# Performance work log

Measured on AMD Instinct MI355X. Metric: run time of the kernel, lower is better.

The kernel has to match this reference:

```python
import math
import jax, jax.numpy as jnp
import numpy as np

B, L, ENC_IN, TFEAT = 32, 1024, 21, 4
DM, EXP = 256, 2
DI = DM * EXP            # 512 d_inner
DST = 64                 # d_state (= configs.d_ff in this repo)
HD = 64                  # headdim
NH = DI // HD            # 8 heads
DC = 4                   # d_conv
NL = 4                   # n_layers
PRED = 192
CO = 21
Q = 64                   # SSD chunk length
DIP = 2 * DI + 2 * DST + NH    # in_proj out dim (z, xBC, dt)
CONVD = DI + 2 * DST           # depthwise-conv channels


def silu(x):
    return x * jax.nn.sigmoid(x)


def positional_embedding(l, d):
    pe = np.zeros((l, d), np.float32)
    pos = np.arange(l, dtype=np.float32)[:, None]
    div = np.exp(np.arange(0, d, 2, dtype=np.float32) * (-math.log(10000.0) / d))
    pe[:, 0::2] = np.sin(pos * div)
    pe[:, 1::2] = np.cos(pos * div)
    return jnp.asarray(pe)


def layernorm(x, g, b):
    m = jnp.mean(x, -1, keepdims=True)
    v = jnp.mean((x - m) ** 2, -1, keepdims=True)
    return (x - m) * jax.lax.rsqrt(v + 1e-5) * g + b


def segsum(x):
    # x: (..., T) -> (..., T, T); out[i,j] = sum_{j<k<=i} x[k], -inf above diagonal
    T = x.shape[-1]
    xx = jnp.broadcast_to(x[..., :, None], (*x.shape, T))
    m1 = jnp.tril(jnp.ones((T, T), bool), -1)
    xs = jnp.cumsum(jnp.where(m1, xx, 0.0), axis=-2)
    m2 = jnp.tril(jnp.ones((T, T), bool), 0)
    return jnp.where(m2, xs, -jnp.inf)


def ssd(X, A, Bm, Cm):
    # chunked SSD (Mamba2). X: (b,l,h,p) = x*dt; A: (b,l,h) = dt*(-exp(A_log)); B,C: (b,l,n)
    b, l, h, p = X.shape
    c = l // Q
    Xc = X.reshape(b, c, Q, h, p)
    Ac = A.reshape(b, c, Q, h).transpose(0, 3, 1, 2)      # (b,h,c,q)
    Bc = Bm.reshape(b, c, Q, -1)
    Cc = Cm.reshape(b, c, Q, -1)
    Acum = jnp.cumsum(Ac, -1)                              # (b,h,c,q)
    Lmat = jnp.exp(segsum(Ac))                             # (b,h,c,q,q)
    Y_diag = jnp.einsum('bcqn,bcsn,bhcqs,bcshp->bcqhp', Cc, Bc, Lmat, Xc)
    decay_states = jnp.exp(Acum[..., -1:] - Acum)          # (b,h,c,q)
    states = jnp.einsum('bcqn,bhcq,bcqhp->bchpn', Bc, decay_states, Xc)
    states = jnp.concatenate([jnp.zeros_like(states[:, :1]), states], axis=1)  # (b,c+1,h,p,n)
    decay_chunk = jnp.exp(segsum(jnp.pad(Acum[..., -1], ((0, 0), (0, 0), (1, 0)))))  # (b,h,c+1,c+1)
    new_states = jnp.einsum('bhzc,bchpn->bzhpn', decay_chunk, states)
    states = new_states[:, :-1]                            # (b,c,h,p,n) entering each chunk
    sdo = jnp.exp(Acum)                                    # (b,h,c,q)
    Y_off = jnp.einsum('bcqn,bchpn,bhcq->bcqhp', Cc, states, sdo)
    return (Y_diag + Y_off).reshape(b, l, h, p)


def mamba2(x, Wi, cw, cb, dtb, Alog, Dp, gw, Wo):
    b, l, _ = x.shape
    zxbcdt = x @ Wi.T                                      # (b,l,DIP)
    z = zxbcdt[..., :DI]
    xBC = zxbcdt[..., DI:DI + CONVD]
    dt = zxbcdt[..., DI + CONVD:]
    # causal depthwise conv (kernel DC) + SiLU
    xp = jnp.pad(xBC, ((0, 0), (DC - 1, 0), (0, 0)))
    xBC = silu(sum(xp[:, k:k + l, :] * cw[:, k] for k in range(DC)) + cb)
    xs = xBC[..., :DI].reshape(b, l, NH, HD)
    Bm = xBC[..., DI:DI + DST]
    Cm = xBC[..., DI + DST:]
    dt = jax.nn.softplus(dt + dtb)                         # (b,l,NH)
    A = -jnp.exp(Alog)                                     # (NH,)
    y = ssd(xs * dt[..., None], dt * A, Bm, Cm) + xs * Dp[:, None]
    y = y.reshape(b, l, DI)
    y = y * silu(z)                                        # gated RMSNorm
    y = y * jax.lax.rsqrt(jnp.mean(y * y, -1, keepdims=True) + 1e-5) * gw
    return y @ Wo.T


def setup_inputs():
    key = jax.random.key(0)
    ks = jax.random.split(key, 16)
    x_enc = jax.random.normal(ks[0], (B, L, ENC_IN), jnp.float32)
    x_mark_enc = jax.random.normal(ks[1], (B, L, TFEAT), jnp.float32)
    x_dec = jax.random.normal(ks[2], (B, 240, ENC_IN), jnp.float32)
    x_mark_dec = jax.random.normal(ks[3], (B, 240, TFEAT), jnp.float32)
    token_w = jax.random.normal(ks[4], (DM, ENC_IN, 3), jnp.float32) * 0.1
    temb_w = jax.random.normal(ks[5], (DM, TFEAT), jnp.float32) * 0.1
    ln_g = jnp.ones((NL, DM), jnp.float32)
    ln_b = jnp.zeros((NL, DM), jnp.float32)
    in_proj_w = jax.random.normal(ks[6], (NL, DIP, DM), jnp.float32) * (DM ** -0.5)
    conv_w = jax.random.normal(ks[7], (NL, CONVD, DC), jnp.float32) * 0.2
    conv_b = jnp.zeros((NL, CONVD), jnp.float32)
    dt_bias = jax.random.normal(ks[8], (NL, NH), jnp.float32) * 0.5
    A_log = jnp.log(jax.random.uniform(ks[9], (NL, NH), jnp.float32, 1.0, 16.0))
    Dskip = jnp.ones((NL, NH), jnp.float32)
    gnorm_w = jnp.ones((NL, DI), jnp.float32)
    out_proj_w = jax.random.normal(ks[10], (NL, DM, DI), jnp.float32) * (DI ** -0.5)
    head_w = jax.random.normal(ks[11], (CO, DM), jnp.float32) * (DM ** -0.5)
    return dict(x_enc=x_enc, x_mark_enc=x_mark_enc, x_dec=x_dec, x_mark_dec=x_mark_dec,
                token_w=token_w, temb_w=temb_w, ln_g=ln_g, ln_b=ln_b,
                in_proj_w=in_proj_w, conv_w=conv_w, conv_b=conv_b, dt_bias=dt_bias,
                A_log=A_log, Dskip=Dskip, gnorm_w=gnorm_w, out_proj_w=out_proj_w,
                head_w=head_w)


def reference(x_enc, x_mark_enc, x_dec, x_mark_dec, token_w, temb_w, ln_g, ln_b,
              in_proj_w, conv_w, conv_b, dt_bias, A_log, Dskip, gnorm_w, out_proj_w, head_w):
    # instance normalization (detached stats)
    mean = jax.lax.stop_gradient(jnp.mean(x_enc, 1, keepdims=True))
    xz = x_enc - mean
    std = jax.lax.stop_gradient(jnp.sqrt(jnp.var(xz, axis=1, keepdims=True) + 1e-5))
    xz = xz / std
    l = xz.shape[1]
    # token embedding: circular-pad Conv1d(enc_in->d_model, k=3)
    xpad = jnp.pad(xz, ((0, 0), (1, 1), (0, 0)), mode='wrap')
    tok = sum(jnp.einsum('blc,dc->bld', xpad[:, k:k + l], token_w[:, :, k]) for k in range(3))
    h = tok + positional_embedding(l, DM)[None] + x_mark_enc @ temb_w.T
    for i in range(NL):
        y = mamba2(h, in_proj_w[i], conv_w[i], conv_b[i], dt_bias[i], A_log[i],
                   Dskip[i], gnorm_w[i], out_proj_w[i])
        h = layernorm(h + y, ln_g[i], ln_b[i])
    out = h @ head_w.T
    out = out * std + mean
    return out[:, -PRED:, :]
```

## Files before the change

### kernel.cpp

```cpp
#include <hip/hip_runtime.h>
#include <hip/hip_bf16.h>


typedef unsigned short ushort_t;
typedef unsigned int uint_t;
typedef __attribute__((ext_vector_type(8))) short short8;
typedef __attribute__((ext_vector_type(4))) float f32x4;
typedef __attribute__((ext_vector_type(4))) ushort_t ushort4_t;

__device__ __forceinline__ float b2f(ushort_t u) {
    uint_t v = ((uint_t)u) << 16;
    return __builtin_bit_cast(float, v);
}
__device__ __forceinline__ ushort_t f2b(float f) {
    uint_t u = __builtin_bit_cast(uint_t, f);
    uint_t r = (u + 0x7FFFu + ((u >> 16) & 1u)) >> 16;
    return (ushort_t)r;
}
__device__ __forceinline__ uint_t cvt_pk2(float a, float b) {
    uint_t r;
    asm("v_cvt_pk_bf16_f32 %0, %1, %2" : "=v"(r) : "v"(a), "v"(b));
    return r;
}
__device__ __forceinline__ float silu_f(float x) {
    return x / (1.f + __expf(-x));
}
__device__ __forceinline__ void gl_lds16(const ushort_t* g, ushort_t* l) {
    __builtin_amdgcn_global_load_lds(
        (const __attribute__((address_space(1))) unsigned int*)g,
        (__attribute__((address_space(3))) unsigned int*)l, 16, 0, 0);
}

__global__ __launch_bounds__(256) void cvt_pad_ip(const float* __restrict__ in,
        ushort_t* __restrict__ out) {
    int i = blockIdx.x * 256 + threadIdx.x;
    if (i >= 4 * 1280 * 256) return;
    int layer = i / (1280 * 256);
    int rem = i - layer * 1280 * 256;
    int n = rem >> 8, k = rem & 255;
    out[i] = (n < 1160) ? f2b(in[(size_t)layer * 1160 * 256 + n * 256 + k]) : (ushort_t)0;
}
__global__ __launch_bounds__(256) void cvt_wop(const float* __restrict__ in,
        const float* __restrict__ gw, ushort_t* __restrict__ out) {
    int i = blockIdx.x * 256 + threadIdx.x;
    int layer = i >> 17;
    int c = i & 511;
    out[i] = f2b(in[i] * gw[layer * 512 + c]);
}
__global__ __launch_bounds__(256) void cvt_convw(const float* __restrict__ in,
        float* __restrict__ out) {
    int i = blockIdx.x * 256 + threadIdx.x;
    if (i >= 10240) return;
    int layer = i / 2560;
    int rem = i - layer * 2560;
    int k = rem / 640, ch = rem - k * 640;
    out[i] = in[layer * 2560 + ch * 4 + k];
}

__global__ __launch_bounds__(256) void pe_kernel(float* __restrict__ pe) {
    int l = blockIdx.x, d = threadIdx.x;
    float div = __expf((float)(d & ~1) * (-9.210340371976184f / 256.0f));
    float arg = (float)l * div;
    pe[l * 256 + d] = (d & 1) ? cosf(arg) : sinf(arg);
}

__global__ __launch_bounds__(256) void stats_kernel(const float* __restrict__ xe,
        float* __restrict__ meanb, float* __restrict__ stdb, float* __restrict__ rstdb) {
    int bi = blockIdx.x;
    int b = bi / 21, c = bi - b * 21;
    int tid = threadIdx.x;
    float s = 0.f, s2 = 0.f;
    for (int l = tid; l < 1024; l += 256) {
        float v = xe[(b * 1024 + l) * 21 + c];
        s += v; s2 += v * v;
    }
    __shared__ float r1[4], r2[4];
    for (int o = 32; o > 0; o >>= 1) { s += __shfl_down(s, o, 64); s2 += __shfl_down(s2, o, 64); }
    if ((tid & 63) == 0) { r1[tid >> 6] = s; r2[tid >> 6] = s2; }
    __syncthreads();
    if (tid == 0) {
        float S = r1[0] + r1[1] + r1[2] + r1[3];
        float S2 = r2[0] + r2[1] + r2[2] + r2[3];
        float m = S * (1.f / 1024.f);
        float var = S2 * (1.f / 1024.f) - m * m;
        float sd = sqrtf(var + 1e-5f);
        meanb[bi] = m; stdb[bi] = sd; rstdb[bi] = 1.f / sd;
    }
}

__global__ __launch_bounds__(256) void embed3_kernel(const float* __restrict__ xe,
        const float* __restrict__ xm, const float* __restrict__ tokw,
        const float* __restrict__ tembw, const float* __restrict__ pe,
        const float* __restrict__ meanb, const float* __restrict__ rstdb,
        float* __restrict__ h, ushort_t* __restrict__ hbf) {
    int blk = blockIdx.x;
    int b = blk >> 4, t = blk & 15;
    int l0 = t * 64;
    int tid = threadIdx.x;
    __shared__ float xw[66][22];
    __shared__ float xmw[64][4];
    __shared__ float mn[21], rs[21];
    if (tid < 21) { mn[tid] = meanb[b * 21 + tid]; rs[tid] = rstdb[b * 21 + tid]; }
    float twr[63];
    {
        const float* tp = tokw + tid * 63;
        #pragma unroll
        for (int i = 0; i < 63; i++) twr[i] = tp[i];
    }
    float tbr[4];
    #pragma unroll
    for (int k = 0; k < 4; k++) tbr[k] = tembw[tid * 4 + k];
    __syncthreads();
    for (int i = tid; i < 1386; i += 256) {
        int row = i / 21, c = i - row * 21;
        int gl = (l0 - 1 + row + 1024) & 1023;
        xw[row][c] = (xe[(size_t)(b * 1024 + gl) * 21 + c] - mn[c]) * rs[c];
    }
    {
        int row = tid >> 2, c = tid & 3;
        xmw[row][c] = xm[(size_t)(b * 1024 + l0 + row) * 4 + c];
    }
    __syncthreads();
    int d = tid;
    float acc2 = 0.f, acc1 = 0.f;
    for (int r = 0; r < 66; r++) {
        float s0 = 0.f, s1 = 0.f, s2 = 0.f;
        #pragma unroll
        for (int c = 0; c < 21; c++) {
            float xv = xw[r][c];
            s0 += xv * twr[c * 3 + 0];
            s1 += xv * twr[c * 3 + 1];
            s2 += xv * twr[c * 3 + 2];
        }
        if (r >= 2) {
            int li = r - 2;
            float acc = acc2 + s2 + pe[(size_t)(l0 + li) * 256 + d];
            #pragma unroll
            for (int k = 0; k < 4; k++) acc += xmw[li][k] * tbr[k];
            size_t o = (size_t)(b * 1024 + l0 + li) * 256 + d;
            h[o] = acc;
            hbf[o] = f2b(acc);
        }
        acc2 = acc1 + s1;
        acc1 = s0;
    }
}

template<int KDIM>
__device__ __forceinline__ void gemm128_main(const ushort_t* __restrict__ Ab,
        const ushort_t* __restrict__ Wb, ushort_t* sA, ushort_t* sW,
        f32x4 (&acc)[16], int m0, int n0) {
    int tid = threadIdx.x;
    int w = tid >> 6, lane = tid & 63;
    int wm = w >> 1, wn = w & 1;
    int rr = lane & 15, quad = lane >> 4;
    int srow0 = w * 32 + (lane >> 2);
    int skk = (lane & 3) * 8;
    int sl0 = w * 1024 + lane * 8;
    for (int k0 = 0; k0 < KDIM; k0 += 64) {
        __syncthreads();
        #pragma unroll
        for (int p = 0; p < 2; p++) {
            #pragma unroll
            for (int j = 0; j < 2; j++) {
                int row = srow0 + j * 16;
                int koff = k0 + p * 32 + skk;
                gl_lds16(Ab + (size_t)(m0 + row) * KDIM + koff, &sA[p * 4096 + sl0 + j * 512]);
                gl_lds16(Wb + (size_t)(n0 + row) * KDIM + koff, &sW[p * 4096 + sl0 + j * 512]);
            }
        }
        __syncthreads();
        #pragma unroll
        for (int p = 0; p < 2; p++) {
            short8 a[4], b[4];
            #pragma unroll
            for (int i = 0; i < 4; i++)
                a[i] = *(const short8*)&sA[p * 4096 + (wm * 64 + i * 16 + rr) * 32 + quad * 8];
            #pragma unroll
            for (int j = 0; j < 4; j++)
                b[j] = *(const short8*)&sW[p * 4096 + (wn * 64 + j * 16 + rr) * 32 + quad * 8];
            #pragma unroll
            for (int i = 0; i < 4; i++)
                #pragma unroll
                for (int j = 0; j < 4; j++)
                    acc[i * 4 + j] = __builtin_amdgcn_mfma_f32_16x16x32_bf16(a[i], b[j], acc[i * 4 + j], 0, 0, 0);
        }
    }
}

__global__ __launch_bounds__(256) void gemm_ip(const ushort_t* __restrict__ A,
        const ushort_t* __restrict__ W, ushort_t* __restrict__ zbuf,
        ushort_t* __restrict__ xbuf) {
    int g = blockIdx.x;
    int xcd = g & 7, s = g >> 3;
    int sq = s / 10;
    int tn = s - sq * 10;
    int tm = (sq << 3) | xcd;
    int m0 = tm * 128, n0 = tn * 128;
    __shared__ ushort_t sA[8192], sW[8192];
    f32x4 acc[16];
    #pragma unroll
    for (int i = 0; i < 16; i++) acc[i] = (f32x4){0.f, 0.f, 0.f, 0.f};
    gemm128_main<256>(A, W, sA, sW, acc, m0, n0);
    int lane = threadIdx.x & 63, w = threadIdx.x >> 6;
    int wm = w >> 1, wn = w & 1;
    int rr = lane & 15, quad = lane >> 4;
    #pragma unroll
    for (int i = 0; i < 4; i++) {
        int mrow = m0 + wm * 64 + i * 16 + quad * 4;
        #pragma unroll
        for (int j = 0; j < 4; j++) {
            int n = n0 + wn * 64 + j * 16 + rr;
            uint_t u01 = cvt_pk2(acc[i * 4 + j][0], acc[i * 4 + j][1]);
            uint_t u23 = cvt_pk2(acc[i * 4 + j][2], acc[i * 4 + j][3]);
            ushort_t vs[4] = {(ushort_t)u01, (ushort_t)(u01 >> 16),
                              (ushort_t)u23, (ushort_t)(u23 >> 16)};
            #pragma unroll
            for (int r2 = 0; r2 < 4; r2++) {
                if (n < 512) zbuf[(size_t)(mrow + r2) * 512 + n] = vs[r2];
                else if (n < 1160) xbuf[(size_t)(mrow + r2) * 704 + (n - 512)] = vs[r2];
            }
        }
    }
}

__global__ __launch_bounds__(256) void gemm_og(const ushort_t* __restrict__ Yb,
        const ushort_t* __restrict__ Zb, const ushort_t* __restrict__ Wb,
        float* __restrict__ h, ushort_t* __restrict__ hbf,
        const float* __restrict__ lng, const float* __restrict__ lnb) {
    int m0 = blockIdx.x * 32;
    int tid = threadIdx.x;
    int w = tid >> 6, lane = tid & 63;
    int wm = w >> 1, wn = w & 1;
    int rr = lane & 15, quad = lane >> 4;
    __shared__ ushort_t sA[2048];
    __shared__ ushort_t sW[16384];
    __shared__ float gssq[32];
    __shared__ float rsum[32][2], rssq[32][2];

    int arow = tid >> 3;
    int akk = (tid & 7) * 8;
    const ushort_t* yrow = Yb + (size_t)(m0 + arow) * 512 + akk;
    const ushort_t* zrow = Zb + (size_t)(m0 + arow) * 512 + akk;
    ushort_t* adst = &sA[((tid & 7) >> 2) * 1024 + arow * 32 + (tid & 3) * 8];

    f32x4 acc[8];
    #pragma unroll
    for (int j = 0; j < 8; j++) acc[j] = (f32x4){0.f, 0.f, 0.f, 0.f};
    float ssqr = 0.f;

    short8 y0 = *(const short8*)(yrow);
    short8 z0 = *(const short8*)(zrow);

    for (int k0 = 0; k0 < 512; k0 += 64) {
        __syncthreads();
        short8 ga;
        {
            uint_t* gau = (uint_t*)&ga;
            #pragma unroll
            for (int jj = 0; jj < 8; jj += 2) {
                float g0 = b2f(((ushort_t*)&y0)[jj]) * silu_f(b2f(((ushort_t*)&z0)[jj]));
                float g1 = b2f(((ushort_t*)&y0)[jj + 1]) * silu_f(b2f(((ushort_t*)&z0)[jj + 1]));
                ssqr += g0 * g0 + g1 * g1;
                gau[jj >> 1] = cvt_pk2(g0, g1);
            }
        }
        *(short8*)adst = ga;
        if (k0 + 64 < 512) {
            y0 = *(const short8*)(yrow + k0 + 64);
            z0 = *(const short8*)(zrow + k0 + 64);
        }
        #pragma unroll
        for (int p = 0; p < 2; p++) {
            #pragma unroll
            for (int j = 0; j < 4; j++)
                gl_lds16(Wb + (size_t)(w * 64 + j * 16 + (lane >> 2)) * 512
                             + k0 + p * 32 + (lane & 3) * 8,
                         &sW[p * 8192 + w * 2048 + j * 512 + lane * 8]);
        }
        __syncthreads();
        #pragma unroll
        for (int p = 0; p < 2; p++) {
            short8 a = *(const short8*)&sA[p * 1024 + (wm * 16 + rr) * 32 + quad * 8];
            #pragma unroll
            for (int j = 0; j < 8; j++) {
                short8 bv = *(const short8*)&sW[p * 8192 + (wn * 128 + j * 16 + rr) * 32 + quad * 8];
                acc[j] = __builtin_amdgcn_mfma_f32_16x16x32_bf16(a, bv, acc[j], 0, 0, 0);
            }
        }
    }

    ssqr += __shfl_xor(ssqr, 1, 64);
    ssqr += __shfl_xor(ssqr, 2, 64);
    ssqr += __shfl_xor(ssqr, 4, 64);
    if ((tid & 7) == 0) gssq[arow] = ssqr;
    __syncthreads();

    float gl[8], bl[8];
    #pragma unroll
    for (int j = 0; j < 8; j++) {
        int col = wn * 128 + j * 16 + rr;
        gl[j] = lng[col]; bl[j] = lnb[col];
    }
    #pragma unroll
    for (int r2 = 0; r2 < 4; r2++) {
        int rowl = wm * 16 + quad * 4 + r2;
        float rmsv = rsqrtf(gssq[rowl] * (1.f / 512.f) + 1e-5f);
        size_t gbase = (size_t)(m0 + rowl) * 256;
        float s = 0.f, s2 = 0.f;
        #pragma unroll
        for (int j = 0; j < 8; j++) {
            int col = wn * 128 + j * 16 + rr;
            float xv = h[gbase + col] + acc[j][r2] * rmsv;
            acc[j][r2] = xv;
            s += xv; s2 += xv * xv;
        }
        #pragma unroll
        for (int o = 1; o < 16; o <<= 1) {
            s += __shfl_xor(s, o, 64);
            s2 += __shfl_xor(s2, o, 64);
        }
        if (rr == 0) { rsum[rowl][wn] = s; rssq[rowl][wn] = s2; }
    }
    __syncthreads();
    #pragma unroll
    for (int r2 = 0; r2 < 4; r2++) {
        int rowl = wm * 16 + quad * 4 + r2;
        float S = rsum[rowl][0] + rsum[rowl][1];
        float S2 = rssq[rowl][0] + rssq[rowl][1];
        float mu = S * (1.f / 256.f);
        float var = S2 * (1.f / 256.f) - mu * mu;
        float rstd = rsqrtf(var + 1e-5f);
        size_t gbase = (size_t)(m0 + rowl) * 256;
        #pragma unroll
        for (int j = 0; j < 8; j++) {
            int col = wn * 128 + j * 16 + rr;
            float o = (acc[j][r2] - mu) * rstd * gl[j] + bl[j];
            h[gbase + col] = o;
            hbf[gbase + col] = f2b(o);
        }
    }
}

__global__ __launch_bounds__(256) void conv_kernel(const ushort_t* __restrict__ xbuf,
        const float* __restrict__ cwt, const float* __restrict__ cb,
        const float* __restrict__ dtb, ushort_t* __restrict__ xc,
        float* __restrict__ dts) {
    if (blockIdx.x >= 2560) {
        int r = (blockIdx.x - 2560) * 256 + threadIdx.x;
        short8 dv = *(const short8*)(xbuf + (size_t)r * 704 + 640);
        #pragma unroll
        for (int j = 0; j < 8; j++) {
            float x = b2f(((ushort_t*)&dv)[j]) + dtb[j];
            dts[(size_t)r * 8 + j] = (x > 20.f) ? x : log1pf(__expf(x));
        }
        return;
    }
    int idx = blockIdx.x * 256 + threadIdx.x;
    int g = idx % 80;
    int rt = idx / 80;
    int ch0 = g * 8;
    int b = rt >> 8;
    int l0 = (rt & 255) << 2;
    float wgt[4][8];
    #pragma unroll
    for (int k = 0; k < 4; k++) {
        float4 w0 = *(const float4*)(cwt + k * 640 + ch0);
        float4 w1 = *(const float4*)(cwt + k * 640 + ch0 + 4);
        wgt[k][0] = w0.x; wgt[k][1] = w0.y; wgt[k][2] = w0.z; wgt[k][3] = w0.w;
        wgt[k][4] = w1.x; wgt[k][5] = w1.y; wgt[k][6] = w1.z; wgt[k][7] = w1.w;
    }
    float bias[8];
    {
        float4 b0 = *(const float4*)(cb + ch0);
        float4 b1 = *(const float4*)(cb + ch0 + 4);
        bias[0] = b0.x; bias[1] = b0.y; bias[2] = b0.z; bias[3] = b0.w;
        bias[4] = b1.x; bias[5] = b1.y; bias[6] = b1.z; bias[7] = b1.w;
    }
    short8 xr[7];
    const ushort_t* base = xbuf + (size_t)(b * 1024 + l0) * 704 + ch0;
    #pragma unroll
    for (int i = 0; i < 7; i++) {
        int ll = l0 - 3 + i;
        if (ll >= 0) xr[i] = *(const short8*)(base + (ptrdiff_t)(i - 3) * 704);
        else         xr[i] = (short8){0, 0, 0, 0, 0, 0, 0, 0};
    }
    #pragma unroll
    for (int lo = 0; lo < 4; lo++) {
        float acc[8];
        #pragma unroll
        for (int j = 0; j < 8; j++) acc[j] = bias[j];
        #pragma unroll
        for (int k = 0; k < 4; k++) {
            #pragma unroll
            for (int j = 0; j < 8; j++)
                acc[j] += b2f(((ushort_t*)&xr[lo + k])[j]) * wgt[k][j];
        }
        short8 o;
        #pragma unroll
        for (int j = 0; j < 8; j++) ((ushort_t*)&o)[j] = f2b(silu_f(acc[j]));
        *(short8*)(xc + (size_t)(b * 1024 + l0 + lo) * 640 + ch0) = o;
    }
}

__global__ __launch_bounds__(256) void ssd_stateA4(const ushort_t* __restrict__ xc,
        const float* __restrict__ dts, const float* __restrict__ alog,
        float* __restrict__ stbuf, float* __restrict__ acbuf) {
    int idx = blockIdx.x;
    int bh = idx >> 2, grp = idx & 3;
    int b = bh >> 3, h = bh & 7;
    float Ah = -__expf(alog[h]);
    int tid = threadIdx.x;
    int q = tid >> 2, pb = (tid & 3) * 16;
    int w = tid >> 6, lane = tid & 63;
    int rr = lane & 15, quad = lane >> 4, qb = w * 16;

    __shared__ ushort_t Bt[64][68], Xt[64][68];
    __shared__ float dec_s[64];
    __shared__ float ad_sh;

    float T[4][4];
    #pragma unroll
    for (int t = 0; t < 4; t++)
        #pragma unroll
        for (int r2 = 0; r2 < 4; r2++) T[t][r2] = 0.f;

    ushort_t bv[16], xv[16];
    float d_pf = 0.f;
    {
        int chunk = grp * 4;
        int l0 = chunk * 64;
        const ushort_t* xrow = xc + (size_t)(b * 1024 + l0 + q) * 640;
        *(short8*)&bv[0] = *(const short8*)(xrow + 512 + pb);
        *(short8*)&bv[8] = *(const short8*)(xrow + 512 + pb + 8);
        *(short8*)&xv[0] = *(const short8*)(xrow + h * 64 + pb);
        *(short8*)&xv[8] = *(const short8*)(xrow + h * 64 + pb + 8);
        if (tid < 64)
            d_pf = dts[(size_t)(b * 1024 + l0 + tid) * 8 + h];
    }

    for (int c4 = 0; c4 < 4; c4++) {
        int chunk = grp * 4 + c4;
        size_t cidx = (size_t)bh * 16 + chunk;
        #pragma unroll
        for (int j = 0; j < 16; j++) Xt[pb + j][q] = xv[j];
        if (tid < 64) {
            float d = d_pf;
            float a = d * Ah;
            #pragma unroll
            for (int off = 1; off < 64; off <<= 1) {
                float t = __shfl_up(a, off, 64);
                if (tid >= off) a += t;
            }
            acbuf[cidx * 64 + tid] = a;
            float tot = __shfl(a, 63, 64);
            dec_s[tid] = __expf(tot - a) * d;
            if (tid == 0) ad_sh = __expf(tot);
        }
        __syncthreads();
        {
            float dq = dec_s[q];
            #pragma unroll
            for (int j = 0; j < 16; j += 2) {
                uint_t u = cvt_pk2(b2f(bv[j]) * dq, b2f(bv[j + 1]) * dq);
                Bt[pb + j][q] = (ushort_t)u;
                Bt[pb + j + 1][q] = (ushort_t)(u >> 16);
            }
        }
        if (c4 < 3) {
            int l0n = (chunk + 1) * 64;
            const ushort_t* xrow = xc + (size_t)(b * 1024 + l0n + q) * 640;
            *(short8*)&bv[0] = *(const short8*)(xrow + 512 + pb);
            *(short8*)&bv[8] = *(const short8*)(xrow + 512 + pb + 8);
            *(short8*)&xv[0] = *(const short8*)(xrow + h * 64 + pb);
            *(short8*)&xv[8] = *(const short8*)(xrow + h * 64 + pb + 8);
            if (tid < 64)
                d_pf = dts[(size_t)(b * 1024 + l0n + tid) * 8 + h];
        }
        __syncthreads();
        f32x4 acc[4];
        #pragma unroll
        for (int t = 0; t < 4; t++) acc[t] = (f32x4){0.f, 0.f, 0.f, 0.f};
        #pragma unroll
        for (int ks = 0; ks < 2; ks++) {
            short8 a = *(const short8*)(&Bt[qb + rr][ks * 32 + quad * 8]);
            #pragma unroll
            for (int t = 0; t < 4; t++) {
                short8 bb = *(const short8*)(&Xt[t * 16 + rr][ks * 32 + quad * 8]);
                acc[t] = __builtin_amdgcn_mfma_f32_16x16x32_bf16(a, bb, acc[t], 0, 0, 0);
            }
        }
        {
            float ad = ad_sh;
            #pragma unroll
            for (int t = 0; t < 4; t++)
                #pragma unroll
                for (int r2 = 0; r2 < 4; r2++)
                    T[t][r2] = ad * T[t][r2] + acc[t][r2];
        }
        __syncthreads();
    }
    float* sb = stbuf + (size_t)idx * 4096;
    #pragma unroll
    for (int t = 0; t < 4; t++) {
        int p = t * 16 + rr;
        #pragma unroll
        for (int r2 = 0; r2 < 4; r2++)
            sb[(qb + quad * 4 + r2) * 64 + p] = T[t][r2];
    }
}

__global__ __launch_bounds__(256) void ssd_outBC4(const ushort_t* __restrict__ xc,
        const float* __restrict__ dts, const float* __restrict__ acbuf,
        const float* __restrict__ dsk, const float* __restrict__ stbuf,
        ushort_t* __restrict__ ybuf) {
    int idx = blockIdx.x;
    int bh = idx >> 2, grp = idx & 3;
    int b = bh >> 3, h = bh & 7;
    float Dh = dsk[h];
    int tid = threadIdx.x;
    int q = tid >> 2, pb = (tid & 3) * 16;
    int w = tid >> 6, lane = tid & 63;
    int rr = lane & 15, quad = lane >> 4, qb = w * 16;

    __shared__ ushort_t Cs[64][68], Bs[64][68], Xt[64][68],
                        Bt[64][68], Shi[64][68], Slo[64][68];
    ushort_t (&Gs)[64][68] = Bs;
    __shared__ float acum_s[64], dtq_s[64], ea_s[64], dec_s[64];
    __shared__ float ad_sh;

    float S[4][4];
    #pragma unroll
    for (int t = 0; t < 4; t++)
        #pragma unroll
        for (int r2 = 0; r2 < 4; r2++) S[t][r2] = 0.f;
    for (int g = 0; g < grp; g++) {
        float Ag = 1.f;
        #pragma unroll
        for (int c = 0; c < 4; c++)
            Ag *= __expf(acbuf[((size_t)bh * 16 + g * 4 + c) * 64 + 63]);
        const float* s0 = stbuf + (size_t)(bh * 4 + g) * 4096;
        #pragma unroll
        for (int t = 0; t < 4; t++) {
            int p = t * 16 + rr;
            #pragma unroll
            for (int r2 = 0; r2 < 4; r2++)
                S[t][r2] = Ag * S[t][r2] + s0[(qb + quad * 4 + r2) * 64 + p];
        }
    }

    ushort_t bv[16], cv[16], xv[16];
    float a_pf = 0.f, d_pf = 0.f;
    {
        int chunk = grp * 4;
        int l0 = chunk * 64;
        const ushort_t* xrow = xc + (size_t)(b * 1024 + l0 + q) * 640;
        *(short8*)&bv[0] = *(const short8*)(xrow + 512 + pb);
        *(short8*)&bv[8] = *(const short8*)(xrow + 512 + pb + 8);
        *(short8*)&cv[0] = *(const short8*)(xrow + 576 + pb);
        *(short8*)&cv[8] = *(const short8*)(xrow + 576 + pb + 8);
        *(short8*)&xv[0] = *(const short8*)(xrow + h * 64 + pb);
        *(short8*)&xv[8] = *(const short8*)(xrow + h * 64 + pb + 8);
        if (tid < 64) {
            size_t cidx = (size_t)bh * 16 + chunk;
            a_pf = acbuf[cidx * 64 + tid];
            d_pf = dts[(size_t)(b * 1024 + l0 + tid) * 8 + h];
        }
    }

    int qq0 = qb + quad * 4;
    for (int c4 = 0; c4 < 4; c4++) {
        int chunk = grp * 4 + c4;
        int l0 = chunk * 64;
        *(short8*)&Bs[q][pb]     = *(const short8*)&bv[0];
        *(short8*)&Bs[q][pb + 8] = *(const short8*)&bv[8];
        *(short8*)&Cs[q][pb]     = *(const short8*)&cv[0];
        *(short8*)&Cs[q][pb + 8] = *(const short8*)&cv[8];
        #pragma unroll
        for (int j = 0; j < 16; j++) Xt[pb + j][q] = xv[j];
        if (tid < 64) {
            float a = a_pf;
            acum_s[tid] = a;
            ea_s[tid] = __expf(a);
            float d = d_pf;
            dtq_s[tid] = d;
            float tot = __shfl(a, 63, 64);
            dec_s[tid] = __expf(tot - a) * d;
            if (tid == 0) ad_sh = __expf(tot);
        }
        #pragma unroll
        for (int t = 0; t < 4; t++) {
            int p = t * 16 + rr;
            uint_t h01 = cvt_pk2(S[t][0], S[t][1]);
            uint_t h23 = cvt_pk2(S[t][2], S[t][3]);
            float l0r = S[t][0] - b2f((ushort_t)h01);
            float l1r = S[t][1] - b2f((ushort_t)(h01 >> 16));
            float l2r = S[t][2] - b2f((ushort_t)h23);
            float l3r = S[t][3] - b2f((ushort_t)(h23 >> 16));
            uint_t lo01 = cvt_pk2(l0r, l1r);
            uint_t lo23 = cvt_pk2(l2r, l3r);
            *(uint2*)&Shi[p][qq0] = make_uint2(h01, h23);
            *(uint2*)&Slo[p][qq0] = make_uint2(lo01, lo23);
        }
        __syncthreads();

        {
            float dq = dec_s[q];
            #pragma unroll
            for (int j = 0; j < 16; j += 2) {
                uint_t u = cvt_pk2(b2f(bv[j]) * dq, b2f(bv[j + 1]) * dq);
                Bt[pb + j][q] = (ushort_t)u;
                Bt[pb + j + 1][q] = (ushort_t)(u >> 16);
            }
        }
        if (c4 < 3) {
            int l0n = (chunk + 1) * 64;
            const ushort_t* xrow = xc + (size_t)(b * 1024 + l0n + q) * 640;
            *(short8*)&bv[0] = *(const short8*)(xrow + 512 + pb);
            *(short8*)&bv[8] = *(const short8*)(xrow + 512 + pb + 8);
            *(short8*)&cv[0] = *(const short8*)(xrow + 576 + pb);
            *(short8*)&cv[8] = *(const short8*)(xrow + 576 + pb + 8);
            *(short8*)&xv[0] = *(const short8*)(xrow + h * 64 + pb);
            *(short8*)&xv[8] = *(const short8*)(xrow + h * 64 + pb + 8);
            if (tid < 64) {
                size_t cidxn = (size_t)bh * 16 + chunk + 1;
                a_pf = acbuf[cidxn * 64 + tid];
                d_pf = dts[(size_t)(b * 1024 + l0n + tid) * 8 + h];
            }
        }
        uint_t gp01[4], gp23[4];
        {
            f32x4 g[4];
            #pragma unroll
            for (int t = 0; t < 4; t++) g[t] = (f32x4){0.f, 0.f, 0.f, 0.f};
            #pragma unroll
            for (int ks = 0; ks < 2; ks++) {
                short8 a = *(const short8*)(&Cs[qb + rr][ks * 32 + quad * 8]);
                #pragma unroll
                for (int t = 0; t < 4; t++) {
                    short8 bb = *(const short8*)(&Bs[t * 16 + rr][ks * 32 + quad * 8]);
                    g[t] = __builtin_amdgcn_mfma_f32_16x16x32_bf16(a, bb, g[t], 0, 0, 0);
                }
            }
            #pragma unroll
            for (int t = 0; t < 4; t++) {
                int s = t * 16 + rr;
                float as = acum_s[s], dss = dtq_s[s];
                float vv[4];
                #pragma unroll
                for (int r2 = 0; r2 < 4; r2++) {
                    int qq = qq0 + r2;
                    vv[r2] = (s <= qq) ? g[t][r2] * __expf(acum_s[qq] - as) * dss : 0.f;
                }
                gp01[t] = cvt_pk2(vv[0], vv[1]);
                gp23[t] = cvt_pk2(vv[2], vv[3]);
            }
        }
        __syncthreads();
        #pragma unroll
        for (int t = 0; t < 4; t++) {
            int s = t * 16 + rr;
            Gs[qq0][s]     = (ushort_t)gp01[t];
            Gs[qq0 + 1][s] = (ushort_t)(gp01[t] >> 16);
            Gs[qq0 + 2][s] = (ushort_t)gp23[t];
            Gs[qq0 + 3][s] = (ushort_t)(gp23[t] >> 16);
        }
        __syncthreads();

        f32x4 aD[4], aO[4];
        #pragma unroll
        for (int t = 0; t < 4; t++) { aD[t] = (f32x4){0.f,0.f,0.f,0.f}; aO[t] = (f32x4){0.f,0.f,0.f,0.f}; }
        #pragma unroll
        for (int ks = 0; ks < 2; ks++) {
            short8 ga = *(const short8*)(&Gs[qb + rr][ks * 32 + quad * 8]);
            short8 ca = *(const short8*)(&Cs[qb + rr][ks * 32 + quad * 8]);
            #pragma unroll
            for (int t = 0; t < 4; t++) {
                short8 xb = *(const short8*)(&Xt[t * 16 + rr][ks * 32 + quad * 8]);
                short8 sh = *(const short8*)(&Shi[t * 16 + rr][ks * 32 + quad * 8]);
                short8 sl = *(const short8*)(&Slo[t * 16 + rr][ks * 32 + quad * 8]);
                aD[t] = __builtin_amdgcn_mfma_f32_16x16x32_bf16(ga, xb, aD[t], 0, 0, 0);
                aO[t] = __builtin_amdgcn_mfma_f32_16x16x32_bf16(ca, sh, aO[t], 0, 0, 0);
                aO[t] = __builtin_amdgcn_mfma_f32_16x16x32_bf16(ca, sl, aO[t], 0, 0, 0);
            }
        }
        {
            f32x4 acc[4];
            #pragma unroll
            for (int t = 0; t < 4; t++) acc[t] = (f32x4){0.f, 0.f, 0.f, 0.f};
            #pragma unroll
            for (int ks = 0; ks < 2; ks++) {
                short8 a = *(const short8*)(&Bt[qb + rr][ks * 32 + quad * 8]);
                #pragma unroll
                for (int t = 0; t < 4; t++) {
                    short8 bb = *(const short8*)(&Xt[t * 16 + rr][ks * 32 + quad * 8]);
                    acc[t] = __builtin_amdgcn_mfma_f32_16x16x32_bf16(a, bb, acc[t], 0, 0, 0);
                }
            }
            #pragma unroll
            for (int t = 0; t < 4; t++) {
                int p = t * 16 + rr;
                float yv[4];
                #pragma unroll
                for (int r2 = 0; r2 < 4; r2++) {
                    int qq = qq0 + r2;
                    yv[r2] = aD[t][r2] + ea_s[qq] * aO[t][r2] + Dh * b2f(Xt[p][qq]);
                }
                uint_t u01 = cvt_pk2(yv[0], yv[1]);
                uint_t u23 = cvt_pk2(yv[2], yv[3]);
                size_t base = (size_t)(b * 1024 + l0 + qq0) * 512 + h * 64 + p;
                ybuf[base]        = (ushort_t)u01;
                ybuf[base + 512]  = (ushort_t)(u01 >> 16);
                ybuf[base + 1024] = (ushort_t)u23;
                ybuf[base + 1536] = (ushort_t)(u23 >> 16);
            }
            float ad = ad_sh;
            #pragma unroll
            for (int t = 0; t < 4; t++)
                #pragma unroll
                for (int r2 = 0; r2 < 4; r2++)
                    S[t][r2] = ad * S[t][r2] + acc[t][r2];
        }
        __syncthreads();
    }
}

__global__ __launch_bounds__(256) void head_kernel(const float* __restrict__ h,
        const float* __restrict__ hw, const float* __restrict__ stdb,
        const float* __restrict__ meanb, float* __restrict__ out) {
    int blk = blockIdx.x;
    int b = blk / 192, t = blk - b * 192;
    int l = 832 + t;
    int tid = threadIdx.x;
    __shared__ float hr[256];
    hr[tid] = h[(size_t)(b * 1024 + l) * 256 + tid];
    __syncthreads();
    if (tid < 21) {
        float acc = 0.f;
        for (int k = 0; k < 256; k++) acc += hr[k] * hw[tid * 256 + k];
        out[(size_t)blk * 21 + tid] = acc * stdb[b * 21 + tid] + meanb[b * 21 + tid];
    }
}

extern "C" void kernel_launch(void* const* d_in, const int* in_sizes, int n_in,
                              void* d_out, int out_size, void* d_ws, size_t ws_size,
                              hipStream_t stream) {
    const float* x_enc  = (const float*)d_in[0];
    const float* x_mark = (const float*)d_in[1];
    const float* tokw   = (const float*)d_in[4];
    const float* tembw  = (const float*)d_in[5];
    const float* ln_g   = (const float*)d_in[6];
    const float* ln_b   = (const float*)d_in[7];
    const float* ipw    = (const float*)d_in[8];
    const float* cw     = (const float*)d_in[9];
    const float* cb     = (const float*)d_in[10];
    const float* dtb    = (const float*)d_in[11];
    const float* alog   = (const float*)d_in[12];
    const float* dsk    = (const float*)d_in[13];
    const float* gw     = (const float*)d_in[14];
    const float* opw    = (const float*)d_in[15];
    const float* hw     = (const float*)d_in[16];
    float* out = (float*)d_out;

    char* w = (char*)d_ws;
    size_t off = 0;
    auto alloc = [&](size_t bytes) -> void* {
        void* p = w + off;
        off += (bytes + 255) & ~(size_t)255;
        return p;
    };
    float* meanb  = (float*)alloc(672 * 4);
    float* stdb   = (float*)alloc(672 * 4);
    float* rstdb  = (float*)alloc(672 * 4);
    float* dts    = (float*)alloc((size_t)262144 * 4);
    float* pebuf  = (float*)alloc((size_t)262144 * 4);
    float* cwt    = (float*)alloc((size_t)10240 * 4);
    float* hbuf   = (float*)alloc((size_t)8388608 * 4);
    ushort_t* hbf = (ushort_t*)alloc((size_t)8388608 * 2);
    ushort_t* zbuf= (ushort_t*)alloc((size_t)32768 * 512 * 2);
    ushort_t* xc  = (ushort_t*)alloc((size_t)32768 * 640 * 2);
    char* R       = (char*)alloc((size_t)71303168);
    ushort_t* ybuf= (ushort_t*)alloc((size_t)32768 * 512 * 2);
    ushort_t* wipb= (ushort_t*)alloc((size_t)4 * 1280 * 256 * 2);
    ushort_t* wopb= (ushort_t*)alloc((size_t)4 * 256 * 512 * 2);
    ushort_t* xbuf = (ushort_t*)R;
    float* stbuf   = (float*)R;
    float* acbuf   = (float*)(R + 67108864);
    (void)ws_size; (void)in_sizes; (void)n_in; (void)out_size;

    stats_kernel<<<672, 256, 0, stream>>>(x_enc, meanb, stdb, rstdb);
    pe_kernel<<<1024, 256, 0, stream>>>(pebuf);
    cvt_pad_ip<<<5120, 256, 0, stream>>>(ipw, wipb);
    cvt_wop<<<2048, 256, 0, stream>>>(opw, gw, wopb);
    cvt_convw<<<40, 256, 0, stream>>>(cw, cwt);
    embed3_kernel<<<512, 256, 0, stream>>>(x_enc, x_mark, tokw, tembw, pebuf,
                                           meanb, rstdb, hbuf, hbf);

    for (int layer = 0; layer < 4; layer++) {
        gemm_ip<<<2560, 256, 0, stream>>>(hbf, wipb + (size_t)layer * 1280 * 256,
                                          zbuf, xbuf);
        conv_kernel<<<2688, 256, 0, stream>>>(xbuf, cwt + layer * 2560,
                                              cb + layer * 640, dtb + layer * 8,
                                              xc, dts);
        ssd_stateA4<<<1024, 256, 0, stream>>>(xc, dts, alog + layer * 8, stbuf, acbuf);
        ssd_outBC4<<<1024, 256, 0, stream>>>(xc, dts, acbuf, dsk + layer * 8,
                                             stbuf, ybuf);
        gemm_og<<<1024, 256, 0, stream>>>(ybuf, zbuf,
                                          wopb + (size_t)layer * 256 * 512,
                                          hbuf, hbf,
                                          ln_g + layer * 256, ln_b + layer * 256);
    }

    head_kernel<<<6144, 256, 0, stream>>>(hbuf, hw, stdb, meanb, out);
}
```

Before: 746.5 us.

## Fuse depthwise causal conv and dt softplus into in_proj GEMM epilogue

The in_proj GEMM now computes the xBC tiles plus a 16-row halo through extra MFMAs. It applies the causal depthwise conv, bias and SiLU from shared memory and writes xc directly, and the dt tile computes softplus in place. This removes the separate conv kernel launch and the global round trip through the intermediate xbuf. In exchange, conv tiles do redundant halo loads and MFMAs, use more LDS and registers, and the blocks become more imbalanced across tile types.

```diff
diff --git a/kernel.cpp b/kernel.cpp
--- a/kernel.cpp
+++ b/kernel.cpp
@@ -146,81 +146,178 @@
     }
 }
 
-template<int KDIM>
-__device__ __forceinline__ void gemm128_main(const ushort_t* __restrict__ Ab,
-        const ushort_t* __restrict__ Wb, ushort_t* sA, ushort_t* sW,
-        f32x4 (&acc)[16], int m0, int n0) {
-    int tid = threadIdx.x;
-    int w = tid >> 6, lane = tid & 63;
-    int wm = w >> 1, wn = w & 1;
-    int rr = lane & 15, quad = lane >> 4;
-    int srow0 = w * 32 + (lane >> 2);
-    int skk = (lane & 3) * 8;
-    int sl0 = w * 1024 + lane * 8;
-    for (int k0 = 0; k0 < KDIM; k0 += 64) {
-        __syncthreads();
-        #pragma unroll
-        for (int p = 0; p < 2; p++) {
-            #pragma unroll
-            for (int j = 0; j < 2; j++) {
-                int row = srow0 + j * 16;
-                int koff = k0 + p * 32 + skk;
-                gl_lds16(Ab + (size_t)(m0 + row) * KDIM + koff, &sA[p * 4096 + sl0 + j * 512]);
-                gl_lds16(Wb + (size_t)(n0 + row) * KDIM + koff, &sW[p * 4096 + sl0 + j * 512]);
-            }
-        }
-        __syncthreads();
-        #pragma unroll
-        for (int p = 0; p < 2; p++) {
-            short8 a[4], b[4];
-            #pragma unroll
-            for (int i = 0; i < 4; i++)
-                a[i] = *(const short8*)&sA[p * 4096 + (wm * 64 + i * 16 + rr) * 32 + quad * 8];
-            #pragma unroll
-            for (int j = 0; j < 4; j++)
-                b[j] = *(const short8*)&sW[p * 4096 + (wn * 64 + j * 16 + rr) * 32 + quad * 8];
-            #pragma unroll
-            for (int i = 0; i < 4; i++)
-                #pragma unroll
-                for (int j = 0; j < 4; j++)
-                    acc[i * 4 + j] = __builtin_amdgcn_mfma_f32_16x16x32_bf16(a[i], b[j], acc[i * 4 + j], 0, 0, 0);
-        }
-    }
-}
-
 __global__ __launch_bounds__(256) void gemm_ip(const ushort_t* __restrict__ A,
-        const ushort_t* __restrict__ W, ushort_t* __restrict__ zbuf,
-        ushort_t* __restrict__ xbuf) {
+        const ushort_t* __restrict__ W, const float* __restrict__ cwt,
+        const float* __restrict__ cb, const float* __restrict__ dtb,
+        ushort_t* __restrict__ zbuf, ushort_t* __restrict__ xc,
+        float* __restrict__ dts) {
     int g = blockIdx.x;
     int xcd = g & 7, s = g >> 3;
     int sq = s / 10;
     int tn = s - sq * 10;
     int tm = (sq << 3) | xcd;
     int m0 = tm * 128, n0 = tn * 128;
-    __shared__ ushort_t sA[8192], sW[8192];
-    f32x4 acc[16];
-    #pragma unroll
-    for (int i = 0; i < 16; i++) acc[i] = (f32x4){0.f, 0.f, 0.f, 0.f};
-    gemm128_main<256>(A, W, sA, sW, acc, m0, n0);
-    int lane = threadIdx.x & 63, w = threadIdx.x >> 6;
+    int l0 = m0 & 1023;
+    bool do_conv = (tn >= 4) && (tn <= 8);
+
+    __shared__ ushort_t smem[18340];
+    ushort_t* sA = smem;
+    ushort_t* sW = smem + 9216;
+
+    int tid = threadIdx.x;
+    int w = tid >> 6, lane = tid & 63;
     int wm = w >> 1, wn = w & 1;
     int rr = lane & 15, quad = lane >> 4;
-    #pragma unroll
-    for (int i = 0; i < 4; i++) {
-        int mrow = m0 + wm * 64 + i * 16 + quad * 4;
+
+    f32x4 acc[16];
+    #pragma unroll
+    for (int i = 0; i < 16; i++) acc[i] = (f32x4){0.f, 0.f, 0.f, 0.f};
+    f32x4 acch[4];
+    #pragma unroll
+    for (int j = 0; j < 4; j++) acch[j] = (f32x4){0.f, 0.f, 0.f, 0.f};
+
+    int srow0 = w * 32 + (lane >> 2);
+    int skk = (lane & 3) * 8;
+    int sl0 = w * 1024 + lane * 8;
+    int hm0 = (l0 > 0) ? m0 - 16 : m0;
+
+    for (int k0 = 0; k0 < 256; k0 += 64) {
+        __syncthreads();
+        #pragma unroll
+        for (int p = 0; p < 2; p++) {
+            int koff = k0 + p * 32 + skk;
+            #pragma unroll
+            for (int j = 0; j < 2; j++) {
+                int row = srow0 + j * 16;
+                gl_lds16(A + (size_t)(m0 + row) * 256 + koff, &sA[p * 4608 + sl0 + j * 512]);
+                gl_lds16(W + (size_t)(n0 + row) * 256 + koff, &sW[p * 4096 + sl0 + j * 512]);
+            }
+            if (do_conv && w == 3)
+                gl_lds16(A + (size_t)(hm0 + (lane >> 2)) * 256 + koff,
+                         &sA[p * 4608 + 4096 + lane * 8]);
+        }
+        __syncthreads();
+        #pragma unroll
+        for (int p = 0; p < 2; p++) {
+            short8 a[4], b[4];
+            #pragma unroll
+            for (int i = 0; i < 4; i++)
+                a[i] = *(const short8*)&sA[p * 4608 + (wm * 64 + i * 16 + rr) * 32 + quad * 8];
+            #pragma unroll
+            for (int j = 0; j < 4; j++)
+                b[j] = *(const short8*)&sW[p * 4096 + (wn * 64 + j * 16 + rr) * 32 + quad * 8];
+            #pragma unroll
+            for (int i = 0; i < 4; i++)
+                #pragma unroll
+                for (int j = 0; j < 4; j++)
+                    acc[i * 4 + j] = __builtin_amdgcn_mfma_f32_16x16x32_bf16(a[i], b[j], acc[i * 4 + j], 0, 0, 0);
+            if (do_conv && wm == 0) {
+                short8 ah = *(const short8*)&sA[p * 4608 + (128 + rr) * 32 + quad * 8];
+                #pragma unroll
+                for (int j = 0; j < 4; j++)
+                    acch[j] = __builtin_amdgcn_mfma_f32_16x16x32_bf16(ah, b[j], acch[j], 0, 0, 0);
+            }
+        }
+    }
+
+    if (tn < 4) {
+        #pragma unroll
+        for (int i = 0; i < 4; i++) {
+            int mrow = m0 + wm * 64 + i * 16 + quad * 4;
+            #pragma unroll
+            for (int j = 0; j < 4; j++) {
+                int n = n0 + wn * 64 + j * 16 + rr;
+                uint_t u01 = cvt_pk2(acc[i * 4 + j][0], acc[i * 4 + j][1]);
+                uint_t u23 = cvt_pk2(acc[i * 4 + j][2], acc[i * 4 + j][3]);
+                zbuf[(size_t)(mrow + 0) * 512 + n] = (ushort_t)u01;
+                zbuf[(size_t)(mrow + 1) * 512 + n] = (ushort_t)(u01 >> 16);
+                zbuf[(size_t)(mrow + 2) * 512 + n] = (ushort_t)u23;
+                zbuf[(size_t)(mrow + 3) * 512 + n] = (ushort_t)(u23 >> 16);
+            }
+        }
+        return;
+    }
+    if (tn == 9) {
+        if (wn == 0 && rr < 8) {
+            float db = dtb[rr];
+            #pragma unroll
+            for (int i = 0; i < 4; i++) {
+                int mrow = m0 + wm * 64 + i * 16 + quad * 4;
+                #pragma unroll
+                for (int r2 = 0; r2 < 4; r2++) {
+                    float x = b2f(f2b(acc[i * 4 + 0][r2])) + db;
+                    dts[(size_t)(mrow + r2) * 8 + rr] = (x > 20.f) ? x : log1pf(__expf(x));
+                }
+            }
+        }
+        return;
+    }
+
+    __syncthreads();
+    ushort_t (*xs)[140] = (ushort_t (*)[140])smem;
+    #pragma unroll
+    for (int i = 0; i < 4; i++)
         #pragma unroll
         for (int j = 0; j < 4; j++) {
-            int n = n0 + wn * 64 + j * 16 + rr;
-            uint_t u01 = cvt_pk2(acc[i * 4 + j][0], acc[i * 4 + j][1]);
-            uint_t u23 = cvt_pk2(acc[i * 4 + j][2], acc[i * 4 + j][3]);
-            ushort_t vs[4] = {(ushort_t)u01, (ushort_t)(u01 >> 16),
-                              (ushort_t)u23, (ushort_t)(u23 >> 16)};
-            #pragma unroll
-            for (int r2 = 0; r2 < 4; r2++) {
-                if (n < 512) zbuf[(size_t)(mrow + r2) * 512 + n] = vs[r2];
-                else if (n < 1160) xbuf[(size_t)(mrow + r2) * 704 + (n - 512)] = vs[r2];
-            }
-        }
+            int col = wn * 64 + j * 16 + rr;
+            #pragma unroll
+            for (int r2 = 0; r2 < 4; r2++)
+                xs[3 + wm * 64 + i * 16 + quad * 4 + r2][col] = f2b(acc[i * 4 + j][r2]);
+        }
+    if (wm == 0 && quad == 3) {
+        #pragma unroll
+        for (int j = 0; j < 4; j++) {
+            int col = wn * 64 + j * 16 + rr;
+            #pragma unroll
+            for (int r2 = 1; r2 < 4; r2++)
+                xs[r2 - 1][col] = (l0 > 0) ? f2b(acch[j][r2]) : (ushort_t)0;
+        }
+    }
+    __syncthreads();
+    int r0 = (tid >> 4) * 8, c0 = (tid & 15) * 8;
+    int ch0 = n0 - 512 + c0;
+    float wgt[4][8], bias[8];
+    #pragma unroll
+    for (int k = 0; k < 4; k++) {
+        float4 w0 = *(const float4*)(cwt + k * 640 + ch0);
+        float4 w1 = *(const float4*)(cwt + k * 640 + ch0 + 4);
+        wgt[k][0] = w0.x; wgt[k][1] = w0.y; wgt[k][2] = w0.z; wgt[k][3] = w0.w;
+        wgt[k][4] = w1.x; wgt[k][5] = w1.y; wgt[k][6] = w1.z; wgt[k][7] = w1.w;
+    }
+    {
+        float4 b0 = *(const float4*)(cb + ch0);
+        float4 b1 = *(const float4*)(cb + ch0 + 4);
+        bias[0] = b0.x; bias[1] = b0.y; bias[2] = b0.z; bias[3] = b0.w;
+        bias[4] = b1.x; bias[5] = b1.y; bias[6] = b1.z; bias[7] = b1.w;
+    }
+    ushort4_t win[4][2];
+    #pragma unroll
+    for (int r = 0; r < 3; r++) {
+        win[r][0] = *(const ushort4_t*)&xs[r0 + r][c0];
+        win[r][1] = *(const ushort4_t*)&xs[r0 + r][c0 + 4];
+    }
+    #pragma unroll
+    for (int m = 0; m < 8; m++) {
+        win[3][0] = *(const ushort4_t*)&xs[r0 + m + 3][c0];
+        win[3][1] = *(const ushort4_t*)&xs[r0 + m + 3][c0 + 4];
+        float o[8];
+        #pragma unroll
+        for (int c = 0; c < 8; c++) {
+            float a = bias[c];
+            #pragma unroll
+            for (int k = 0; k < 4; k++)
+                a += b2f(((const ushort_t*)&win[k][c >> 2])[c & 3]) * wgt[k][c];
+            o[c] = a;
+        }
+        short8 ov;
+        uint_t* ovu = (uint_t*)&ov;
+        #pragma unroll
+        for (int c = 0; c < 8; c += 2)
+            ovu[c >> 1] = cvt_pk2(silu_f(o[c]), silu_f(o[c + 1]));
+        *(short8*)(xc + (size_t)(m0 + r0 + m) * 640 + ch0) = ov;
+        win[0][0] = win[1][0]; win[0][1] = win[1][1];
+        win[1][0] = win[2][0]; win[1][1] = win[2][1];
+        win[2][0] = win[3][0]; win[2][1] = win[3][1];
     }
 }
 
@@ -339,67 +436,6 @@
             h[gbase + col] = o;
             hbf[gbase + col] = f2b(o);
         }
-    }
-}
-
-__global__ __launch_bounds__(256) void conv_kernel(const ushort_t* __restrict__ xbuf,
-        const float* __restrict__ cwt, const float* __restrict__ cb,
-        const float* __restrict__ dtb, ushort_t* __restrict__ xc,
-        float* __restrict__ dts) {
-    if (blockIdx.x >= 2560) {
-        int r = (blockIdx.x - 2560) * 256 + threadIdx.x;
-        short8 dv = *(const short8*)(xbuf + (size_t)r * 704 + 640);
-        #pragma unroll
-        for (int j = 0; j < 8; j++) {
-            float x = b2f(((ushort_t*)&dv)[j]) + dtb[j];
-            dts[(size_t)r * 8 + j] = (x > 20.f) ? x : log1pf(__expf(x));
-        }
-        return;
-    }
-    int idx = blockIdx.x * 256 + threadIdx.x;
-    int g = idx % 80;
-    int rt = idx / 80;
-    int ch0 = g * 8;
-    int b = rt >> 8;
-    int l0 = (rt & 255) << 2;
-    float wgt[4][8];
-    #pragma unroll
-    for (int k = 0; k < 4; k++) {
-        float4 w0 = *(const float4*)(cwt + k * 640 + ch0);
-        float4 w1 = *(const float4*)(cwt + k * 640 + ch0 + 4);
-        wgt[k][0] = w0.x; wgt[k][1] = w0.y; wgt[k][2] = w0.z; wgt[k][3] = w0.w;
-        wgt[k][4] = w1.x; wgt[k][5] = w1.y; wgt[k][6] = w1.z; wgt[k][7] = w1.w;
-    }
-    float bias[8];
-    {
-        float4 b0 = *(const float4*)(cb + ch0);
-        float4 b1 = *(const float4*)(cb + ch0 + 4);
-        bias[0] = b0.x; bias[1] = b0.y; bias[2] = b0.z; bias[3] = b0.w;
-        bias[4] = b1.x; bias[5] = b1.y; bias[6] = b1.z; bias[7] = b1.w;
-    }
-    short8 xr[7];
-    const ushort_t* base = xbuf + (size_t)(b * 1024 + l0) * 704 + ch0;
-    #pragma unroll
-    for (int i = 0; i < 7; i++) {
-        int ll = l0 - 3 + i;
-        if (ll >= 0) xr[i] = *(const short8*)(base + (ptrdiff_t)(i - 3) * 704);
-        else         xr[i] = (short8){0, 0, 0, 0, 0, 0, 0, 0};
-    }
-    #pragma unroll
-    for (int lo = 0; lo < 4; lo++) {
-        float acc[8];
-        #pragma unroll
-        for (int j = 0; j < 8; j++) acc[j] = bias[j];
-        #pragma unroll
-        for (int k = 0; k < 4; k++) {
-            #pragma unroll
-            for (int j = 0; j < 8; j++)
-                acc[j] += b2f(((ushort_t*)&xr[lo + k])[j]) * wgt[k][j];
-        }
-        short8 o;
-        #pragma unroll
-        for (int j = 0; j < 8; j++) ((ushort_t*)&o)[j] = f2b(silu_f(acc[j]));
-        *(short8*)(xc + (size_t)(b * 1024 + l0 + lo) * 640 + ch0) = o;
     }
 }
 
@@ -783,7 +819,6 @@
     ushort_t* ybuf= (ushort_t*)alloc((size_t)32768 * 512 * 2);
     ushort_t* wipb= (ushort_t*)alloc((size_t)4 * 1280 * 256 * 2);
     ushort_t* wopb= (ushort_t*)alloc((size_t)4 * 256 * 512 * 2);
-    ushort_t* xbuf = (ushort_t*)R;
     float* stbuf   = (float*)R;
     float* acbuf   = (float*)(R + 67108864);
     (void)ws_size; (void)in_sizes; (void)n_in; (void)out_size;
@@ -798,10 +833,8 @@
 
     for (int layer = 0; layer < 4; layer++) {
         gemm_ip<<<2560, 256, 0, stream>>>(hbf, wipb + (size_t)layer * 1280 * 256,
-                                          zbuf, xbuf);
-        conv_kernel<<<2688, 256, 0, stream>>>(xbuf, cwt + layer * 2560,
-                                              cb + layer * 640, dtb + layer * 8,
-                                              xc, dts);
+                                          cwt + layer * 2560, cb + layer * 640,
+                                          dtb + layer * 8, zbuf, xc, dts);
         ssd_stateA4<<<1024, 256, 0, stream>>>(xc, dts, alog + layer * 8, stbuf, acbuf);
         ssd_outBC4<<<1024, 256, 0, stream>>>(xc, dts, acbuf, dsk + layer * 8,
                                              stbuf, ybuf);
```

Result: slower. 841.1 us (+12.7%).
